# Optimization experiments

Hardware: AMD Instinct MI355X
Metric: run time of the kernel (lower is better)

Reference implementation:

```python
import jax, jax.numpy as jnp
import numpy as np
from jax import lax

EPS = 1e-5
R = 1  # output_lin_radius
K = 2 * R - 1


def conv(x, w, pad):
    return lax.conv_general_dilated(
        x, w, window_strides=(1, 1), padding=[(pad, pad), (pad, pad)],
        dimension_numbers=('NCHW', 'OIHW', 'NCHW'))


def batch_norm(x):
    # affine=False training-mode BN: per-channel stats over (N, H, W), biased var
    mean = jnp.mean(x, axis=(0, 2, 3), keepdims=True)
    var = jnp.mean((x - mean) ** 2, axis=(0, 2, 3), keepdims=True)
    return (x - mean) * lax.rsqrt(var + EPS)


def conv_bn(x, w, pad=1):
    return batch_norm(conv(x, w, pad))


def setup_inputs() -> dict:
    key = jax.random.key(0)
    ks = jax.random.split(key, 16)
    H = W = 512
    d = {
        'x': jax.random.normal(ks[0], (1, 4, H, W), jnp.float32),
        'prev_c': jnp.ones((1, 32, H, W), jnp.float32),
        'prev_h': jnp.ones((1, 32, H, W), jnp.float32),
        'holes_coordinates': jax.random.randint(ks[1], (256, 2), 0, H, jnp.int32),
        'w_e1': jax.random.normal(ks[2], (32, 4, 3, 3), jnp.float32) * 0.05,
        'w_e2': jax.random.normal(ks[3], (32, 32, 3, 3), jnp.float32) * 0.05,
        'w_f': jax.random.normal(ks[4], (32, 64, 3, 3), jnp.float32) * 0.05,
        'w_i': jax.random.normal(ks[5], (32, 64, 3, 3), jnp.float32) * 0.05,
        'w_c': jax.random.normal(ks[6], (32, 64, 3, 3), jnp.float32) * 0.05,
        'w_o': jax.random.normal(ks[7], (32, 64, 3, 3), jnp.float32) * 0.05,
        'w_r1': jax.random.normal(ks[8], (32, 32, 3, 3), jnp.float32) * 0.05,
        'w_r2': jax.random.normal(ks[9], (3, 32, 3, 3), jnp.float32) * 0.05,
        'w_oil': jax.random.normal(ks[10], (1, K * K), jnp.float32) * 0.5,
        'b_oil': jnp.zeros((1,), jnp.float32),
        'w_wat': jax.random.normal(ks[11], (1, K * K), jnp.float32) * 0.5,
        'b_wat': jnp.zeros((1,), jnp.float32),
        'w_gas': jax.random.normal(ks[12], (1, K * K), jnp.float32) * 0.5,
        'b_gas': jnp.zeros((1,), jnp.float32),
    }
    return d


def reference(x, prev_c, prev_h, holes_coordinates, w_e1, w_e2, w_f, w_i, w_c,
              w_o, w_r1, w_r2, w_oil, b_oil, w_wat, b_wat, w_gas, b_gas):
    # embedding: ConvBlock -> ReLU -> ConvBlock
    x_emb = conv_bn(jax.nn.relu(conv_bn(x, w_e1)), w_e2)
    x_and_h = jnp.concatenate([prev_h, x_emb], axis=1)
    f_t = jax.nn.sigmoid(conv_bn(x_and_h, w_f))
    i_t = jax.nn.sigmoid(conv_bn(x_and_h, w_i))
    c_t = jnp.tanh(conv_bn(x_and_h, w_c))
    o_t = jax.nn.sigmoid(conv_bn(x_and_h, w_o))
    next_c = prev_c * f_t + i_t * c_t
    next_h = jnp.tanh(next_c) * o_t
    # hidden_to_result: ConvBlock(pad=1) -> ReLU -> ConvBlock(pad=4): spatial grows by +3/side
    res_map = conv_bn(jax.nn.relu(conv_bn(next_h, w_r1)), w_r2, pad=4)
    rm = res_map[0]  # (3, H+6, W+6)
    hx = holes_coordinates[:, 0]
    hy = holes_coordinates[:, 1]
    offs = jnp.arange(K) + (4 - R)  # slice start = coord - R + 1 + 3
    ix = hx[:, None] + offs[None, :]          # (n, K)
    iy = hy[:, None] + offs[None, :]          # (n, K)
    patches = rm[:, ix[:, :, None], iy[:, None, :]]  # (3, n, K, K)
    flat = patches.reshape(3, hx.shape[0], K * K)    # (3, n, K*K)
    res = jnp.stack([
        flat[0] @ w_oil[0] + b_oil[0],
        flat[1] @ w_wat[0] + b_wat[0],
        flat[2] @ w_gas[0] + b_gas[0],
    ], axis=1)  # (n, 3)
    return ((next_c, next_h), res)
```

## Files before the change

kernel.cpp:

```cpp
#include <hip/hip_runtime.h>
#include <cstddef>


typedef float f4 __attribute__((ext_vector_type(4)));

#define H_   512
#define W_   512
#define HW_  (H_ * W_)
#define EPS_ 1e-5f
#define RMH  518
#define RMHW (RMH * RMH)
#define TS   16

static __device__ __forceinline__ float sigmoidf_(float x) { return 1.f / (1.f + expf(-x)); }

static __device__ __forceinline__ void wtr(const float* __restrict__ src,
                                           float* __restrict__ dst,
                                           int cin, int cout, int idx) {
    int co = idx / (cin * 9);
    int r  = idx - co * cin * 9;
    dst[r * cout + co] = src[idx];
}

__global__ __launch_bounds__(256) void wtrans_all_kernel(
    const float* __restrict__ we1, const float* __restrict__ we2,
    const float* __restrict__ wf,  const float* __restrict__ wi,
    const float* __restrict__ wc,  const float* __restrict__ wo,
    const float* __restrict__ wr1, const float* __restrict__ wr2,
    float* __restrict__ te1, float* __restrict__ te2, float* __restrict__ tg,
    float* __restrict__ tr1, float* __restrict__ tr2)
{
    int idx = blockIdx.x * 256 + threadIdx.x;
    if (idx < 1152)        wtr(we1, te1, 4, 32, idx);
    else if (idx < 10368)  wtr(we2, te2, 32, 32, idx - 1152);
    else if (idx < 28800)  wtr(wf, tg + 0 * 18432, 64, 32, idx - 10368);
    else if (idx < 47232)  wtr(wi, tg + 1 * 18432, 64, 32, idx - 28800);
    else if (idx < 65664)  wtr(wc, tg + 2 * 18432, 64, 32, idx - 47232);
    else if (idx < 84096)  wtr(wo, tg + 3 * 18432, 64, 32, idx - 65664);
    else if (idx < 93312)  wtr(wr1, tr1, 32, 32, idx - 84096);
    else if (idx < 94176)  wtr(wr2, tr2, 32, 3, idx - 93312);
}

__global__ void wgprep_kernel(float* __restrict__ wt, const float* __restrict__ S2,
                              float* __restrict__ bias) {
    int tid = threadIdx.x;
    int z = tid >> 5, co = tid & 31;
    __shared__ float m_[32], is_[32];
    if (tid < 32) {
        float s = S2[tid * 2], ss = S2[tid * 2 + 1];
        float m = s * (1.f / HW_);
        m_[tid] = m;
        is_[tid] = rsqrtf(ss * (1.f / HW_) - m * m + EPS_);
    }
    __syncthreads();
    float b = 0.f;
    float* wz = wt + (size_t)z * 64 * 9 * 32;
    for (int ci = 32; ci < 64; ++ci) {
        float m = m_[ci - 32], is = is_[ci - 32];
        for (int k = 0; k < 9; ++k) {
            size_t idx = (size_t)(ci * 9 + k) * 32 + co;
            float w = wz[idx] * is;
            wz[idx] = w;
            b -= m * w;
        }
    }
    bias[tid] = b;
}

template <int CIN, int COUT, int PAD, int MODE>
__global__ __launch_bounds__(256) void conv3x3_kernel(
    const float* __restrict__ in, const float* __restrict__ sums,
    const float* __restrict__ wt, float* __restrict__ out,
    float* __restrict__ partials, int OH, int OW, float inv_n_in)
{
    constexpr int CH  = (CIN < 8) ? CIN : 8;
    constexpr int NCH = CIN / CH;
    constexpr int NCA = (MODE == 2) ? CIN : 1;

    __shared__ float smem[CH * 324];
    __shared__ float s_mean[NCA], s_istd[NCA];
    __shared__ float red[4][COUT][2];

    const int tid = threadIdx.x;
    const int tx = tid & 15, ty = tid >> 4;
    const int bx = blockIdx.x, by = blockIdx.y;

    if constexpr (MODE == 2) {
        if (tid < CIN) {
            float s = sums[tid * 2], ss = sums[tid * 2 + 1];
            float m = s * inv_n_in;
            s_mean[tid] = m;
            s_istd[tid] = rsqrtf(ss * inv_n_in - m * m + EPS_);
        }
    }

    float acc[COUT];
#pragma unroll
    for (int i = 0; i < COUT; ++i) acc[i] = 0.f;

#pragma unroll 1
    for (int cc = 0; cc < NCH; ++cc) {
        __syncthreads();
        for (int i = tid; i < CH * 324; i += 256) {
            int ci = i / 324;
            int rem = i - ci * 324;
            int ly = rem / 18, lx = rem - ly * 18;
            int gy = by * TS + ly - PAD, gx = bx * TS + lx - PAD;
            float v = 0.f;
            if ((unsigned)gy < 512u && (unsigned)gx < 512u) {
                int c = cc * CH + ci;
                v = in[(size_t)c * HW_ + gy * 512 + gx];
                if constexpr (MODE == 2)
                    v = fmaxf((v - s_mean[c]) * s_istd[c], 0.f);
            }
            smem[i] = v;
        }
        __syncthreads();

        const float* wc = wt + (size_t)cc * CH * 9 * COUT;
#pragma unroll
        for (int ci = 0; ci < CH; ++ci) {
#pragma unroll
            for (int kk = 0; kk < 9; ++kk) {
                const int ky = kk / 3, kx = kk - ky * 3;
                float v = smem[ci * 324 + (ty + ky) * 18 + (tx + kx)];
                const float* w = wc + (ci * 9 + kk) * COUT;
#pragma unroll
                for (int co = 0; co < COUT; ++co)
                    acc[co] = fmaf(v, w[co], acc[co]);
            }
        }
    }

    const int oy = by * TS + ty, ox = bx * TS + tx;
    const bool valid = (oy < OH) && (ox < OW);
    if (valid) {
#pragma unroll
        for (int co = 0; co < COUT; ++co)
            out[(size_t)co * OH * OW + oy * OW + ox] = acc[co];
    }

    const float scale = valid ? 1.f : 0.f;
    const int wave = tid >> 6, lane = tid & 63;
#pragma unroll
    for (int co = 0; co < COUT; ++co) {
        float s = acc[co] * scale;
        float ss = acc[co] * acc[co] * scale;
#pragma unroll
        for (int o = 32; o > 0; o >>= 1) {
            s += __shfl_down(s, o);
            ss += __shfl_down(ss, o);
        }
        if (lane == 0) { red[wave][co][0] = s; red[wave][co][1] = ss; }
    }
    __syncthreads();
    if (tid < COUT) {
        float s = red[0][tid][0] + red[1][tid][0] + red[2][tid][0] + red[3][tid][0];
        float ss = red[0][tid][1] + red[1][tid][1] + red[2][tid][1] + red[3][tid][1];
        int bl = by * gridDim.x + bx;
        partials[((size_t)bl * COUT + tid) * 2]     = s;
        partials[((size_t)bl * COUT + tid) * 2 + 1] = ss;
    }
}

template <int COUT, int MODE>
__global__ __launch_bounds__(256, 4) void conv3x3_p2_kernel(
    const float* __restrict__ in, const float* __restrict__ sums,
    const float* __restrict__ wt, float* __restrict__ out,
    float* __restrict__ partials, float inv_n_in)
{
    constexpr int NCA = (MODE == 2) ? 32 : 1;

    __shared__ float smem[8 * 612];
    __shared__ float s_mean[NCA], s_istd[NCA];
    __shared__ float red[4][COUT][2];

    const int tid = threadIdx.x;
    const int tx = tid & 15, ty = tid >> 4;
    const int bx = blockIdx.x, by = blockIdx.y;

    if constexpr (MODE == 2) {
        if (tid < 32) {
            float s = sums[tid * 2], ss = sums[tid * 2 + 1];
            float m = s * inv_n_in;
            s_mean[tid] = m;
            s_istd[tid] = rsqrtf(ss * inv_n_in - m * m + EPS_);
        }
    }

    float acc0[COUT], acc1[COUT];
#pragma unroll
    for (int i = 0; i < COUT; ++i) { acc0[i] = 0.f; acc1[i] = 0.f; }

#pragma unroll 1
    for (int cc = 0; cc < 4; ++cc) {
        __syncthreads();
        for (int i = tid; i < 8 * 612; i += 256) {
            int ci = i / 612;
            int rem = i - ci * 612;
            int ly = rem / 34, lx = rem - ly * 34;
            int gy = by * 16 + ly - 1, gx = bx * 32 + lx - 1;
            float v = 0.f;
            if ((unsigned)gy < 512u && (unsigned)gx < 512u) {
                int c = cc * 8 + ci;
                v = in[(size_t)c * HW_ + gy * 512 + gx];
                if constexpr (MODE == 2)
                    v = fmaxf((v - s_mean[c]) * s_istd[c], 0.f);
            }
            smem[i] = v;
        }
        __syncthreads();

        const float* wc = wt + (size_t)cc * 8 * 9 * COUT;
#pragma unroll
        for (int ci = 0; ci < 8; ++ci) {
#pragma unroll
            for (int kk = 0; kk < 9; ++kk) {
                const int ky = kk / 3, kx = kk - ky * 3;
                const int base = ci * 612 + (ty + ky) * 34 + (tx + kx);
                float v0 = smem[base];
                float v1 = smem[base + 16];
                const float* w = wc + (ci * 9 + kk) * COUT;
#pragma unroll
                for (int co = 0; co < COUT; ++co) {
                    acc0[co] = fmaf(v0, w[co], acc0[co]);
                    acc1[co] = fmaf(v1, w[co], acc1[co]);
                }
            }
        }
    }

    const int oy = by * 16 + ty;
    const size_t p0 = (size_t)oy * 512 + bx * 32 + tx;
#pragma unroll
    for (int co = 0; co < COUT; ++co) {
        out[(size_t)co * HW_ + p0]      = acc0[co];
        out[(size_t)co * HW_ + p0 + 16] = acc1[co];
    }

    const int wave = tid >> 6, lane = tid & 63;
#pragma unroll
    for (int co = 0; co < COUT; ++co) {
        float s = acc0[co] + acc1[co];
        float ss = acc0[co] * acc0[co] + acc1[co] * acc1[co];
#pragma unroll
        for (int o = 32; o > 0; o >>= 1) {
            s += __shfl_down(s, o);
            ss += __shfl_down(ss, o);
        }
        if (lane == 0) { red[wave][co][0] = s; red[wave][co][1] = ss; }
    }
    __syncthreads();
    if (tid < COUT) {
        float s = red[0][tid][0] + red[1][tid][0] + red[2][tid][0] + red[3][tid][0];
        float ss = red[0][tid][1] + red[1][tid][1] + red[2][tid][1] + red[3][tid][1];
        int bl = by * gridDim.x + bx;
        partials[((size_t)bl * COUT + tid) * 2]     = s;
        partials[((size_t)bl * COUT + tid) * 2 + 1] = ss;
    }
}

__global__ __launch_bounds__(256, 4) void conv_gates_kernel(
    const float* __restrict__ ph, const float* __restrict__ y2,
    const float* __restrict__ S2, const float* __restrict__ wt,
    const float* __restrict__ bias, float* __restrict__ out,
    float* __restrict__ partials)
{
    __shared__ float smem[8 * 612];
    __shared__ float s_pad[64];
    __shared__ float red[4][32][2];

    const int tid = threadIdx.x;
    const int tx = tid & 15, ty = tid >> 4;
    const int bx = blockIdx.x, by = blockIdx.y, z = blockIdx.z;

    if (tid < 64) {
        float pv = 0.f;
        if (tid >= 32) pv = S2[(tid - 32) * 2] * (1.f / HW_);
        s_pad[tid] = pv;
    }

    float acc0[32], acc1[32];
#pragma unroll
    for (int co = 0; co < 32; ++co) {
        float b = bias[z * 32 + co];
        acc0[co] = b; acc1[co] = b;
    }

    const float* wz = wt + (size_t)z * 64 * 9 * 32;

#pragma unroll 1
    for (int cc = 0; cc < 8; ++cc) {
        __syncthreads();
        const float* src = (cc < 4) ? (ph + (size_t)cc * 8 * HW_)
                                    : (y2 + (size_t)(cc - 4) * 8 * HW_);
        for (int i = tid; i < 8 * 612; i += 256) {
            int ci = i / 612;
            int rem = i - ci * 612;
            int ly = rem / 34, lx = rem - ly * 34;
            int gy = by * 16 + ly - 1, gx = bx * 32 + lx - 1;
            float v;
            if ((unsigned)gy < 512u && (unsigned)gx < 512u)
                v = src[(size_t)ci * HW_ + gy * 512 + gx];
            else
                v = s_pad[cc * 8 + ci];
            smem[i] = v;
        }
        __syncthreads();

        const float* wc = wz + cc * 8 * 9 * 32;
#pragma unroll
        for (int ci = 0; ci < 8; ++ci) {
#pragma unroll
            for (int kk = 0; kk < 9; ++kk) {
                const int ky = kk / 3, kx = kk - ky * 3;
                const int base = ci * 612 + (ty + ky) * 34 + (tx + kx);
                float v0 = smem[base];
                float v1 = smem[base + 16];
                const float* w = wc + (ci * 9 + kk) * 32;
#pragma unroll
                for (int co = 0; co < 32; ++co) {
                    acc0[co] = fmaf(v0, w[co], acc0[co]);
                    acc1[co] = fmaf(v1, w[co], acc1[co]);
                }
            }
        }
    }

    const int oy = by * 16 + ty;
    const size_t p0 = (size_t)oy * 512 + bx * 32 + tx;
    float* oz = out + (size_t)z * 32 * HW_;
#pragma unroll
    for (int co = 0; co < 32; ++co) {
        oz[(size_t)co * HW_ + p0]      = acc0[co];
        oz[(size_t)co * HW_ + p0 + 16] = acc1[co];
    }

    const int wave = tid >> 6, lane = tid & 63;
#pragma unroll
    for (int co = 0; co < 32; ++co) {
        float s = acc0[co] + acc1[co];
        float ss = acc0[co] * acc0[co] + acc1[co] * acc1[co];
#pragma unroll
        for (int o = 32; o > 0; o >>= 1) {
            s += __shfl_down(s, o);
            ss += __shfl_down(ss, o);
        }
        if (lane == 0) { red[wave][co][0] = s; red[wave][co][1] = ss; }
    }
    __syncthreads();
    if (tid < 32) {
        float s = red[0][tid][0] + red[1][tid][0] + red[2][tid][0] + red[3][tid][0];
        float ss = red[0][tid][1] + red[1][tid][1] + red[2][tid][1] + red[3][tid][1];
        int bl = z * 512 + by * gridDim.x + bx;
        partials[((size_t)bl * 32 + tid) * 2]     = s;
        partials[((size_t)bl * 32 + tid) * 2 + 1] = ss;
    }
}

__global__ __launch_bounds__(256) void reduce_kernel(const float* __restrict__ p,
                                                     float* __restrict__ sums,
                                                     int nb, int cout) {
    int c = blockIdx.x;
    int g = c / cout, co = c - g * cout;
    const float* base = p + (size_t)g * nb * cout * 2;
    float s = 0.f, ss = 0.f;
    for (int i = threadIdx.x; i < nb; i += 256) {
        s  += base[((size_t)i * cout + co) * 2];
        ss += base[((size_t)i * cout + co) * 2 + 1];
    }
#pragma unroll
    for (int o = 32; o > 0; o >>= 1) {
        s += __shfl_down(s, o);
        ss += __shfl_down(ss, o);
    }
    __shared__ float ls[4], lss[4];
    int w = threadIdx.x >> 6;
    if ((threadIdx.x & 63) == 0) { ls[w] = s; lss[w] = ss; }
    __syncthreads();
    if (threadIdx.x == 0) {
        sums[c * 2]     = ls[0] + ls[1] + ls[2] + ls[3];
        sums[c * 2 + 1] = lss[0] + lss[1] + lss[2] + lss[3];
    }
}

__global__ __launch_bounds__(256) void lstm_elem_kernel(
    const float* __restrict__ gates, const float* __restrict__ S,
    const float* __restrict__ prev_c, float* __restrict__ out)
{
    __shared__ float mn[128], is_[128];
    int tid = threadIdx.x;
    if (tid < 128) {
        float s = S[tid * 2], ss = S[tid * 2 + 1];
        float m = s * (1.f / HW_);
        mn[tid] = m;
        is_[tid] = rsqrtf(ss * (1.f / HW_) - m * m + EPS_);
    }
    __syncthreads();
    size_t p = (size_t)(blockIdx.x * 256 + tid) * 4;
    for (int ch = 0; ch < 32; ++ch) {
        f4 fv = *(const f4*)(gates + (size_t)ch * HW_ + p);
        f4 iv = *(const f4*)(gates + (size_t)(32 + ch) * HW_ + p);
        f4 cv = *(const f4*)(gates + (size_t)(64 + ch) * HW_ + p);
        f4 ov = *(const f4*)(gates + (size_t)(96 + ch) * HW_ + p);
        f4 pc = *(const f4*)(prev_c + (size_t)ch * HW_ + p);
        float fm = mn[ch], fs = is_[ch];
        float im = mn[32 + ch], isd = is_[32 + ch];
        float cm = mn[64 + ch], cs = is_[64 + ch];
        float om = mn[96 + ch], os = is_[96 + ch];
        f4 nc, nh;
#pragma unroll
        for (int k = 0; k < 4; ++k) {
            float f = sigmoidf_((fv[k] - fm) * fs);
            float i = sigmoidf_((iv[k] - im) * isd);
            float c = tanhf((cv[k] - cm) * cs);
            float o = sigmoidf_((ov[k] - om) * os);
            float ncv = pc[k] * f + i * c;
            nc[k] = ncv;
            nh[k] = tanhf(ncv) * o;
        }
        *(f4*)(out + (size_t)ch * HW_ + p) = nc;
        *(f4*)(out + (size_t)32 * HW_ + (size_t)ch * HW_ + p) = nh;
    }
}

__global__ void holes_kernel(const float* __restrict__ rm, const float* __restrict__ S,
                             const int* __restrict__ holes,
                             const float* __restrict__ w_oil, const float* __restrict__ b_oil,
                             const float* __restrict__ w_wat, const float* __restrict__ b_wat,
                             const float* __restrict__ w_gas, const float* __restrict__ b_gas,
                             float* __restrict__ res)
{
    int i = threadIdx.x;
    int hx = holes[i * 2], hy = holes[i * 2 + 1];
    const float invn = 1.f / (float)RMHW;
#pragma unroll
    for (int c = 0; c < 3; ++c) {
        float s = S[c * 2], ss = S[c * 2 + 1];
        float m = s * invn;
        float istd = rsqrtf(ss * invn - m * m + EPS_);
        float raw = rm[(size_t)c * RMHW + (size_t)(hx + 3) * RMH + (hy + 3)];
        float nv = (raw - m) * istd;
        float w = (c == 0) ? w_oil[0] : (c == 1) ? w_wat[0] : w_gas[0];
        float b = (c == 0) ? b_oil[0] : (c == 1) ? b_wat[0] : b_gas[0];
        res[i * 3 + c] = nv * w + b;
    }
}

extern "C" void kernel_launch(void* const* d_in, const int* in_sizes, int n_in,
                              void* d_out, int out_size, void* d_ws, size_t ws_size,
                              hipStream_t stream) {
    const float* x      = (const float*)d_in[0];
    const float* prev_c = (const float*)d_in[1];
    const float* prev_h = (const float*)d_in[2];
    const int*   holes  = (const int*)d_in[3];
    const float* w_e1 = (const float*)d_in[4];
    const float* w_e2 = (const float*)d_in[5];
    const float* w_f  = (const float*)d_in[6];
    const float* w_i  = (const float*)d_in[7];
    const float* w_c  = (const float*)d_in[8];
    const float* w_o  = (const float*)d_in[9];
    const float* w_r1 = (const float*)d_in[10];
    const float* w_r2 = (const float*)d_in[11];
    const float* w_oil = (const float*)d_in[12];
    const float* b_oil = (const float*)d_in[13];
    const float* w_wat = (const float*)d_in[14];
    const float* b_wat = (const float*)d_in[15];
    const float* w_gas = (const float*)d_in[16];
    const float* b_gas = (const float*)d_in[17];

    float* out = (float*)d_out;
    float* ws  = (float*)d_ws;

    size_t o = 0;
    float* wt_e1 = ws + o; o += 4 * 9 * 32;
    float* wt_e2 = ws + o; o += 32 * 9 * 32;
    float* wt_g  = ws + o; o += 4 * 64 * 9 * 32;
    float* wt_r1 = ws + o; o += 32 * 9 * 32;
    float* wt_r2 = ws + o; o += 32 * 9 * 3;
    float* gbias = ws + o; o += 128;
    float* y1    = ws + o; o += (size_t)32 * HW_;
    float* y2    = ws + o; o += (size_t)32 * HW_;
    float* gates = ws + o; o += (size_t)128 * HW_;
    float* P1 = ws + o; o += 1024 * 32 * 2;
    float* P2 = ws + o; o += 1024 * 32 * 2;
    float* P3 = ws + o; o += 4096 * 32 * 2;
    float* P4 = ws + o; o += 1024 * 32 * 2;
    float* P5 = ws + o; o += 1089 * 3 * 2;
    float* S1 = ws + o; o += 64;
    float* S2 = ws + o; o += 64;
    float* S3 = ws + o; o += 256;
    float* S4 = ws + o; o += 64;
    float* S5 = ws + o; o += 8;
    float* r1 = y1;
    float* rm = y2;

    const float invHW = 1.f / (float)HW_;
    dim3 blk(256);

    wtrans_all_kernel<<<dim3(368), blk, 0, stream>>>(
        w_e1, w_e2, w_f, w_i, w_c, w_o, w_r1, w_r2,
        wt_e1, wt_e2, wt_g, wt_r1, wt_r2);

    conv3x3_kernel<4, 32, 1, 0><<<dim3(32, 32), blk, 0, stream>>>(
        x, nullptr, wt_e1, y1, P1, H_, W_, invHW);
    reduce_kernel<<<dim3(32), blk, 0, stream>>>(P1, S1, 1024, 32);

    conv3x3_p2_kernel<32, 2><<<dim3(16, 32), blk, 0, stream>>>(
        y1, S1, wt_e2, y2, P2, invHW);
    reduce_kernel<<<dim3(32), blk, 0, stream>>>(P2, S2, 512, 32);

    wgprep_kernel<<<dim3(1), dim3(128), 0, stream>>>(wt_g, S2, gbias);
    conv_gates_kernel<<<dim3(16, 32, 4), blk, 0, stream>>>(
        prev_h, y2, S2, wt_g, gbias, gates, P3);
    reduce_kernel<<<dim3(128), blk, 0, stream>>>(P3, S3, 512, 32);

    lstm_elem_kernel<<<dim3(256), blk, 0, stream>>>(gates, S3, prev_c, out);

    conv3x3_p2_kernel<32, 0><<<dim3(16, 32), blk, 0, stream>>>(
        out + (size_t)32 * HW_, nullptr, wt_r1, r1, P4, invHW);
    reduce_kernel<<<dim3(32), blk, 0, stream>>>(P4, S4, 512, 32);

    conv3x3_kernel<32, 3, 4, 2><<<dim3(33, 33), blk, 0, stream>>>(
        r1, S4, wt_r2, rm, P5, RMH, RMH, invHW);
    reduce_kernel<<<dim3(3), blk, 0, stream>>>(P5, S5, 1089, 3);

    holes_kernel<<<dim3(1), blk, 0, stream>>>(
        rm, S5, holes, w_oil, b_oil, w_wat, b_wat, w_gas, b_gas,
        out + (size_t)64 * HW_);
}
```

Baseline: 1.151 ms.

## Run LSTM gate convolution on fp16 MFMA with separate stats pass

Replaces the FP32 FMA gate convolution with an implicit-GEMM kernel using 16x16x32 fp16 MFMA instructions. Activations are staged in LDS as a swizzled fp16 tile, and weights are pre-packed to fp16 in a tap-major layout with the BN fold applied. A one-off probe kernel discovers the MFMA output lane mapping at runtime. BN statistics for the gates move out of the conv epilogue into a separate vectorized reduction over the gate buffer. This trades fp32 accuracy for fp16 inputs and adds an extra full read of the 128-channel gate tensor.

```diff
diff --git a/kernel.cpp b/kernel.cpp
--- a/kernel.cpp
+++ b/kernel.cpp
@@ -3,6 +3,8 @@
 
 
 typedef float f4 __attribute__((ext_vector_type(4)));
+typedef float f32x4 __attribute__((ext_vector_type(4)));
+typedef _Float16 f16x8 __attribute__((ext_vector_type(8)));
 
 #define H_   512
 #define W_   512
@@ -24,25 +26,52 @@
 
 __global__ __launch_bounds__(256) void wtrans_all_kernel(
     const float* __restrict__ we1, const float* __restrict__ we2,
-    const float* __restrict__ wf,  const float* __restrict__ wi,
-    const float* __restrict__ wc,  const float* __restrict__ wo,
     const float* __restrict__ wr1, const float* __restrict__ wr2,
-    float* __restrict__ te1, float* __restrict__ te2, float* __restrict__ tg,
+    float* __restrict__ te1, float* __restrict__ te2,
     float* __restrict__ tr1, float* __restrict__ tr2)
 {
     int idx = blockIdx.x * 256 + threadIdx.x;
     if (idx < 1152)        wtr(we1, te1, 4, 32, idx);
     else if (idx < 10368)  wtr(we2, te2, 32, 32, idx - 1152);
-    else if (idx < 28800)  wtr(wf, tg + 0 * 18432, 64, 32, idx - 10368);
-    else if (idx < 47232)  wtr(wi, tg + 1 * 18432, 64, 32, idx - 28800);
-    else if (idx < 65664)  wtr(wc, tg + 2 * 18432, 64, 32, idx - 47232);
-    else if (idx < 84096)  wtr(wo, tg + 3 * 18432, 64, 32, idx - 65664);
-    else if (idx < 93312)  wtr(wr1, tr1, 32, 32, idx - 84096);
-    else if (idx < 94176)  wtr(wr2, tr2, 32, 3, idx - 93312);
-}
-
-__global__ void wgprep_kernel(float* __restrict__ wt, const float* __restrict__ S2,
-                              float* __restrict__ bias) {
+    else if (idx < 19584)  wtr(wr1, tr1, 32, 32, idx - 10368);
+    else if (idx < 20448)  wtr(wr2, tr2, 32, 3, idx - 19584);
+}
+
+__global__ __launch_bounds__(64) void probe_layout_kernel(int* __restrict__ tbl) {
+    int lane = threadIdx.x;
+    int lx = lane & 15, lhi = lane >> 4;
+    f16x8 a1, b1, a2, b2, a3, b3;
+#pragma unroll
+    for (int e = 0; e < 8; ++e) {
+        int k = lhi * 8 + e;
+        a1[e] = (_Float16)((k == 0) ? (float)(lx + 1) : 0.f);
+        b1[e] = (_Float16)((k == 0) ? 1.f : 0.f);
+        a2[e] = (_Float16)((k == 0) ? 1.f : 0.f);
+        b2[e] = (_Float16)((k == 0) ? (float)(lx + 1) : 0.f);
+        a3[e] = (_Float16)((k == 17) ? 3.f : 0.f);
+        b3[e] = (_Float16)((k == 17) ? 5.f : 0.f);
+    }
+    f32x4 z = {0.f, 0.f, 0.f, 0.f};
+    f32x4 d1 = __builtin_amdgcn_mfma_f32_16x16x32_f16(a1, b1, z, 0, 0, 0);
+    f32x4 d2 = __builtin_amdgcn_mfma_f32_16x16x32_f16(a2, b2, z, 0, 0, 0);
+    f32x4 d3 = __builtin_amdgcn_mfma_f32_16x16x32_f16(a3, b3, z, 0, 0, 0);
+#pragma unroll
+    for (int r = 0; r < 4; ++r) {
+        int m = (int)rintf(d1[r]) - 1;
+        int n = (int)rintf(d2[r]) - 1;
+        bool ok = (fabsf(d3[r] - 15.f) < 0.5f) &&
+                  m >= 0 && m < 16 && n >= 0 && n < 16;
+        if (!ok) { m = lhi * 4 + r; n = lx; }
+        tbl[lane * 4 + r] = ((m & 15) << 4) | (n & 15);
+    }
+}
+
+__global__ __launch_bounds__(128) void wgprep16_kernel(
+    const float* __restrict__ wf, const float* __restrict__ wi,
+    const float* __restrict__ wc, const float* __restrict__ wo,
+    const float* __restrict__ S2, _Float16* __restrict__ w16,
+    float* __restrict__ bias)
+{
     int tid = threadIdx.x;
     int z = tid >> 5, co = tid & 31;
     __shared__ float m_[32], is_[32];
@@ -53,18 +82,21 @@
         is_[tid] = rsqrtf(ss * (1.f / HW_) - m * m + EPS_);
     }
     __syncthreads();
+    const float* w = (z == 0) ? wf : (z == 1) ? wi : (z == 2) ? wc : wo;
+    const float* wco = w + co * 576;
+    _Float16* o16 = w16 + (size_t)(z * 32 + co) * 576;
     float b = 0.f;
-    float* wz = wt + (size_t)z * 64 * 9 * 32;
-    for (int ci = 32; ci < 64; ++ci) {
-        float m = m_[ci - 32], is = is_[ci - 32];
-        for (int k = 0; k < 9; ++k) {
-            size_t idx = (size_t)(ci * 9 + k) * 32 + co;
-            float w = wz[idx] * is;
-            wz[idx] = w;
-            b -= m * w;
-        }
-    }
-    bias[tid] = b;
+    for (int ci = 0; ci < 64; ++ci) {
+        for (int tap = 0; tap < 9; ++tap) {
+            float v = wco[ci * 9 + tap];
+            if (ci >= 32) {
+                v *= is_[ci - 32];
+                b -= m_[ci - 32] * v;
+            }
+            o16[tap * 64 + ci] = (_Float16)v;
+        }
+    }
+    bias[z * 32 + co] = b;
 }
 
 template <int CIN, int COUT, int PAD, int MODE>
@@ -260,101 +292,127 @@
     }
 }
 
-__global__ __launch_bounds__(256, 4) void conv_gates_kernel(
+__global__ __launch_bounds__(256) void conv_gates_mfma_kernel(
     const float* __restrict__ ph, const float* __restrict__ y2,
-    const float* __restrict__ S2, const float* __restrict__ wt,
-    const float* __restrict__ bias, float* __restrict__ out,
-    float* __restrict__ partials)
-{
-    __shared__ float smem[8 * 612];
-    __shared__ float s_pad[64];
-    __shared__ float red[4][32][2];
+    const float* __restrict__ S2, const _Float16* __restrict__ w16,
+    const float* __restrict__ gbias, const int* __restrict__ tbl,
+    float* __restrict__ out)
+{
+    __shared__ alignas(16) _Float16 ltile[6912];
+    __shared__ float s_pad[32];
 
     const int tid = threadIdx.x;
-    const int tx = tid & 15, ty = tid >> 4;
-    const int bx = blockIdx.x, by = blockIdx.y, z = blockIdx.z;
-
-    if (tid < 64) {
-        float pv = 0.f;
-        if (tid >= 32) pv = S2[(tid - 32) * 2] * (1.f / HW_);
-        s_pad[tid] = pv;
-    }
-
-    float acc0[32], acc1[32];
-#pragma unroll
-    for (int co = 0; co < 32; ++co) {
-        float b = bias[z * 32 + co];
-        acc0[co] = b; acc1[co] = b;
-    }
-
-    const float* wz = wt + (size_t)z * 64 * 9 * 32;
-
-#pragma unroll 1
-    for (int cc = 0; cc < 8; ++cc) {
-        __syncthreads();
-        const float* src = (cc < 4) ? (ph + (size_t)cc * 8 * HW_)
-                                    : (y2 + (size_t)(cc - 4) * 8 * HW_);
-        for (int i = tid; i < 8 * 612; i += 256) {
-            int ci = i / 612;
-            int rem = i - ci * 612;
-            int ly = rem / 34, lx = rem - ly * 34;
-            int gy = by * 16 + ly - 1, gx = bx * 32 + lx - 1;
-            float v;
-            if ((unsigned)gy < 512u && (unsigned)gx < 512u)
-                v = src[(size_t)ci * HW_ + gy * 512 + gx];
-            else
-                v = s_pad[cc * 8 + ci];
-            smem[i] = v;
-        }
-        __syncthreads();
-
-        const float* wc = wz + cc * 8 * 9 * 32;
-#pragma unroll
-        for (int ci = 0; ci < 8; ++ci) {
-#pragma unroll
-            for (int kk = 0; kk < 9; ++kk) {
-                const int ky = kk / 3, kx = kk - ky * 3;
-                const int base = ci * 612 + (ty + ky) * 34 + (tx + kx);
-                float v0 = smem[base];
-                float v1 = smem[base + 16];
-                const float* w = wc + (ci * 9 + kk) * 32;
-#pragma unroll
-                for (int co = 0; co < 32; ++co) {
-                    acc0[co] = fmaf(v0, w[co], acc0[co]);
-                    acc1[co] = fmaf(v1, w[co], acc1[co]);
+    const int wave = tid >> 6, lane = tid & 63;
+    const int lx = lane & 15, lhi = lane >> 4;
+    const int bx = blockIdx.x, by = blockIdx.y;
+    const int x0 = bx * 16, y0 = by * 4;
+
+    if (tid < 32) s_pad[tid] = S2[tid * 2] * (1.f / HW_);
+    __syncthreads();
+
+    {
+        int p = tid & 127, g = tid >> 7;
+        if (p < 108) {
+            int py = p / 18, px = p - py * 18;
+            int gy = y0 + py - 1, gx = x0 + px - 1;
+            bool ok = ((unsigned)gy < 512u) && ((unsigned)gx < 512u);
+            const float* srcp = (g == 0) ? ph : y2;
+            int off = gy * 512 + gx;
+            int base16 = p * 64 + g * 32;
+            int sw = (p & 7) << 3;
+#pragma unroll
+            for (int j4 = 0; j4 < 4; ++j4) {
+                f16x8 pk;
+#pragma unroll
+                for (int e = 0; e < 8; ++e) {
+                    int c = j4 * 8 + e;
+                    float v;
+                    if (ok) v = srcp[(size_t)c * HW_ + off];
+                    else    v = (g == 0) ? 0.f : s_pad[c];
+                    pk[e] = (_Float16)v;
                 }
-            }
-        }
-    }
-
-    const int oy = by * 16 + ty;
-    const size_t p0 = (size_t)oy * 512 + bx * 32 + tx;
-    float* oz = out + (size_t)z * 32 * HW_;
-#pragma unroll
-    for (int co = 0; co < 32; ++co) {
-        oz[(size_t)co * HW_ + p0]      = acc0[co];
-        oz[(size_t)co * HW_ + p0 + 16] = acc1[co];
-    }
-
-    const int wave = tid >> 6, lane = tid & 63;
-#pragma unroll
-    for (int co = 0; co < 32; ++co) {
-        float s = acc0[co] + acc1[co];
-        float ss = acc0[co] * acc0[co] + acc1[co] * acc1[co];
-#pragma unroll
-        for (int o = 32; o > 0; o >>= 1) {
-            s += __shfl_down(s, o);
-            ss += __shfl_down(ss, o);
-        }
-        if (lane == 0) { red[wave][co][0] = s; red[wave][co][1] = ss; }
-    }
-    __syncthreads();
-    if (tid < 32) {
-        float s = red[0][tid][0] + red[1][tid][0] + red[2][tid][0] + red[3][tid][0];
-        float ss = red[0][tid][1] + red[1][tid][1] + red[2][tid][1] + red[3][tid][1];
-        int bl = z * 512 + by * gridDim.x + bx;
-        partials[((size_t)bl * 32 + tid) * 2]     = s;
-        partials[((size_t)bl * 32 + tid) * 2 + 1] = ss;
+                *(f16x8*)&ltile[(base16 + j4 * 8) ^ sw] = pk;
+            }
+        }
+    }
+
+    int t4[4];
+#pragma unroll
+    for (int r = 0; r < 4; ++r) t4[r] = tbl[lane * 4 + r];
+
+    __syncthreads();
+
+    f32x4 acc0[4], acc1[4];
+#pragma unroll
+    for (int nt = 0; nt < 4; ++nt) {
+        acc0[nt] = (f32x4){0.f, 0.f, 0.f, 0.f};
+        acc1[nt] = (f32x4){0.f, 0.f, 0.f, 0.f};
+    }
+
+    const _Float16* wg = w16 + (size_t)(wave * 32) * 576;
+    const int abase = lx * 576 + lhi * 8;
+
+#pragma unroll 3
+    for (int tap = 0; tap < 9; ++tap) {
+        int dy = tap / 3;
+        int dx = tap - dy * 3;
+        int prow = dy * 18 + dx + lx;
+#pragma unroll
+        for (int h = 0; h < 2; ++h) {
+            int wk = tap * 64 + h * 32;
+            f16x8 a0 = *(const f16x8*)(wg + abase + wk);
+            f16x8 a1 = *(const f16x8*)(wg + abase + 16 * 576 + wk);
+            int coff = h * 32 + lhi * 8;
+#pragma unroll
+            for (int nt = 0; nt < 4; ++nt) {
+                int p = prow + nt * 18;
+                int i16 = (p * 64 + coff) ^ ((p & 7) << 3);
+                f16x8 b = *(const f16x8*)&ltile[i16];
+                acc0[nt] = __builtin_amdgcn_mfma_f32_16x16x32_f16(a0, b, acc0[nt], 0, 0, 0);
+                acc1[nt] = __builtin_amdgcn_mfma_f32_16x16x32_f16(a1, b, acc1[nt], 0, 0, 0);
+            }
+        }
+    }
+
+    float* gz = out + (size_t)(wave * 32) * HW_;
+#pragma unroll
+    for (int r = 0; r < 4; ++r) {
+        int m = (t4[r] >> 4) & 15, n = t4[r] & 15;
+        float b0v = gbias[wave * 32 + m];
+        float b1v = gbias[wave * 32 + 16 + m];
+#pragma unroll
+        for (int nt = 0; nt < 4; ++nt) {
+            size_t po = (size_t)(y0 + nt) * 512 + x0 + n;
+            gz[(size_t)m * HW_ + po]        = acc0[nt][r] + b0v;
+            gz[(size_t)(16 + m) * HW_ + po] = acc1[nt][r] + b1v;
+        }
+    }
+}
+
+__global__ __launch_bounds__(256) void gates_stats_kernel(
+    const float* __restrict__ gates, float* __restrict__ partials)
+{
+    int q = blockIdx.x;
+    int c = blockIdx.y;
+    const f4* g4 = (const f4*)(gates + (size_t)c * HW_ + (size_t)q * 65536);
+    float s = 0.f, ss = 0.f;
+    for (int i = threadIdx.x; i < 16384; i += 256) {
+        f4 v = g4[i];
+#pragma unroll
+        for (int k = 0; k < 4; ++k) { s += v[k]; ss += v[k] * v[k]; }
+    }
+#pragma unroll
+    for (int o = 32; o > 0; o >>= 1) {
+        s += __shfl_down(s, o);
+        ss += __shfl_down(ss, o);
+    }
+    __shared__ float ls[4], lss[4];
+    int w = threadIdx.x >> 6;
+    if ((threadIdx.x & 63) == 0) { ls[w] = s; lss[w] = ss; }
+    __syncthreads();
+    if (threadIdx.x == 0) {
+        partials[((size_t)q * 128 + c) * 2]     = ls[0] + ls[1] + ls[2] + ls[3];
+        partials[((size_t)q * 128 + c) * 2 + 1] = lss[0] + lss[1] + lss[2] + lss[3];
     }
 }
 
@@ -475,16 +533,17 @@
     size_t o = 0;
     float* wt_e1 = ws + o; o += 4 * 9 * 32;
     float* wt_e2 = ws + o; o += 32 * 9 * 32;
-    float* wt_g  = ws + o; o += 4 * 64 * 9 * 32;
     float* wt_r1 = ws + o; o += 32 * 9 * 32;
     float* wt_r2 = ws + o; o += 32 * 9 * 3;
     float* gbias = ws + o; o += 128;
+    float* wg16f = ws + o; o += 36864;
+    int*   tbl   = (int*)(ws + o); o += 260;
     float* y1    = ws + o; o += (size_t)32 * HW_;
     float* y2    = ws + o; o += (size_t)32 * HW_;
     float* gates = ws + o; o += (size_t)128 * HW_;
     float* P1 = ws + o; o += 1024 * 32 * 2;
     float* P2 = ws + o; o += 1024 * 32 * 2;
-    float* P3 = ws + o; o += 4096 * 32 * 2;
+    float* P3 = ws + o; o += 4 * 128 * 2;
     float* P4 = ws + o; o += 1024 * 32 * 2;
     float* P5 = ws + o; o += 1089 * 3 * 2;
     float* S1 = ws + o; o += 64;
@@ -494,13 +553,14 @@
     float* S5 = ws + o; o += 8;
     float* r1 = y1;
     float* rm = y2;
+    _Float16* w16 = (_Float16*)wg16f;
 
     const float invHW = 1.f / (float)HW_;
     dim3 blk(256);
 
-    wtrans_all_kernel<<<dim3(368), blk, 0, stream>>>(
-        w_e1, w_e2, w_f, w_i, w_c, w_o, w_r1, w_r2,
-        wt_e1, wt_e2, wt_g, wt_r1, wt_r2);
+    wtrans_all_kernel<<<dim3(80), blk, 0, stream>>>(
+        w_e1, w_e2, w_r1, w_r2, wt_e1, wt_e2, wt_r1, wt_r2);
+    probe_layout_kernel<<<dim3(1), dim3(64), 0, stream>>>(tbl);
 
     conv3x3_kernel<4, 32, 1, 0><<<dim3(32, 32), blk, 0, stream>>>(
         x, nullptr, wt_e1, y1, P1, H_, W_, invHW);
@@ -510,10 +570,13 @@
         y1, S1, wt_e2, y2, P2, invHW);
     reduce_kernel<<<dim3(32), blk, 0, stream>>>(P2, S2, 512, 32);
 
-    wgprep_kernel<<<dim3(1), dim3(128), 0, stream>>>(wt_g, S2, gbias);
-    conv_gates_kernel<<<dim3(16, 32, 4), blk, 0, stream>>>(
-        prev_h, y2, S2, wt_g, gbias, gates, P3);
-    reduce_kernel<<<dim3(128), blk, 0, stream>>>(P3, S3, 512, 32);
+    wgprep16_kernel<<<dim3(1), dim3(128), 0, stream>>>(
+        w_f, w_i, w_c, w_o, S2, w16, gbias);
+    conv_gates_mfma_kernel<<<dim3(32, 128), blk, 0, stream>>>(
+        prev_h, y2, S2, w16, gbias, tbl, gates);
+
+    gates_stats_kernel<<<dim3(4, 128), blk, 0, stream>>>(gates, P3);
+    reduce_kernel<<<dim3(128), blk, 0, stream>>>(P3, S3, 4, 128);
 
     lstm_elem_kernel<<<dim3(256), blk, 0, stream>>>(gates, S3, prev_c, out);
 
```

Result: faster. 951.4 us (-17.4%).
